# Optimization experiments

Hardware: AMD Instinct MI355X
Metric: run time of the kernel (lower is better)

## Reference

```python
import jax, jax.numpy as jnp
import numpy as np

NEG = -1e9

def mask_from_lens(src_lens, lip_lens, Tx, Ty):
    # [B, Tx, Ty] valid mask
    mx = jnp.arange(Tx)[None, :] < src_lens[:, None]
    my = jnp.arange(Ty)[None, :] < lip_lens[:, None]
    return (mx[:, :, None] & my[:, None, :]).astype(jnp.float32)

def maximum_path(value, mask):
    # Monotonic alignment search (VITS-style). value, mask: [B, Tx, Ty]
    B, Tx, Ty = value.shape
    value = value * mask
    xr = jnp.arange(Tx)[None, :]

    def fwd(v, inp):
        val_j, j = inp
        v0 = jnp.concatenate([jnp.full((B, 1), NEG, value.dtype), v[:, :-1]], axis=1)
        stay = v >= v0                      # True: best prev is same x
        vmax = jnp.where(stay, v, v0)
        vnew = jnp.where(xr <= j, vmax + val_j, NEG)
        return vnew, stay

    val_T = jnp.transpose(value, (2, 0, 1))          # [Ty,B,Tx]
    _, dirs = jax.lax.scan(fwd, jnp.zeros((B, Tx), value.dtype),
                           (val_T, jnp.arange(Ty)))
    mask_T = jnp.transpose(mask, (2, 0, 1)) > 0
    dirs = jnp.where(mask_T, dirs, True)             # padded cols: stay

    idx0 = mask[:, :, 0].sum(1).astype(jnp.int32) - 1  # src_lens - 1
    br = jnp.arange(B)

    def bwd(index, dir_j):
        onehot = jax.nn.one_hot(index, Tx, dtype=value.dtype)
        d = dir_j[br, index]
        return index + d.astype(jnp.int32) - 1, onehot

    _, path = jax.lax.scan(bwd, idx0, dirs, reverse=True)  # [Ty,B,Tx]
    return jnp.transpose(path, (1, 2, 0)) * mask

def setup_inputs() -> dict:
    key = jax.random.key(0)
    k1, k2, k3, k4, k5 = jax.random.split(key, 5)
    B, Ts, Tl, D = 32, 512, 2048, 256
    lip_motion_embedding = jax.random.normal(k1, (B, Tl, D), jnp.float32)
    output_phoneme = jax.random.normal(k2, (B, Ts, D), jnp.float32)
    src_lens = jax.random.randint(k3, (B,), Ts // 2, Ts + 1, jnp.int32)
    lip_lens = jax.random.randint(k4, (B,), Tl // 2, Tl + 1, jnp.int32)
    d_targets = jax.random.randint(k5, (B, Ts), 1, 8, jnp.int32)
    d_targets = jnp.where(jnp.arange(Ts)[None, :] < src_lens[:, None], d_targets, 0)
    return {"lip_motion_embedding": lip_motion_embedding,
            "output_phoneme": output_phoneme,
            "d_targets": d_targets,
            "src_lens": src_lens,
            "lip_lens": lip_lens}

def reference(lip_motion_embedding, output_phoneme, d_targets, src_lens, lip_lens):
    B, Tl, D = lip_motion_embedding.shape
    Ts = output_phoneme.shape[1]

    # mean expansion coefficient
    mean_cof = (d_targets.sum(-1) / lip_lens).mean()

    # normalized similarity  [B, Ts, Tl]
    norm_lip = lip_motion_embedding / jnp.linalg.norm(lip_motion_embedding, axis=2, keepdims=True)
    text_norm_base = jnp.linalg.norm(output_phoneme, axis=2, keepdims=True)
    norm_text = jnp.nan_to_num(output_phoneme / (text_norm_base + 1), nan=1.0)
    similarity = jnp.einsum('bld,bsd->bsl', norm_lip, norm_text)

    # duration targets rescaled to lip frame rate
    cofs = d_targets.sum(1) / lip_lens                      # [B]
    lip_targets = jnp.round(d_targets / cofs[:, None])      # [B, Ts] float
    dif = lip_lens.astype(lip_targets.dtype) - lip_targets.sum(1)
    max_idx = jnp.argmax(lip_targets, axis=1)
    lip_targets = lip_targets.at[jnp.arange(B), max_idx].add(dif)

    # gt_similarity: contiguous segments of ones per phoneme (vectorized scatter)
    lt = lip_targets.astype(jnp.int32)
    ends = jnp.cumsum(lt, axis=1)                           # [B, Ts]
    begins = ends - lt
    kk = jnp.arange(Tl)[None, None, :]
    gt_similarity = ((kk >= begins[:, :, None]) & (kk < ends[:, :, None])).astype(similarity.dtype)

    mask_sim = mask_from_lens(src_lens, lip_lens, Ts, Tl)
    alignment = maximum_path(similarity, mask_sim)
    d_predictions = jax.lax.stop_gradient(alignment.sum(-1)) * mean_cof

    return similarity, gt_similarity, alignment, d_predictions
```

## Files before the change

### kernel.cpp

```cpp
#include <hip/hip_runtime.h>
#include <math.h>

#define BATCH 32
#define TS    512
#define TL    2048
#define DD    256
#define NEGV  -1e9f

#define SIM_OFF   ((size_t)0)
#define GT_OFF    ((size_t)BATCH*TS*TL)
#define ALIGN_OFF ((size_t)2*BATCH*TS*TL)
#define DPRED_OFF ((size_t)3*BATCH*TS*TL)

#define WS_MEAN   0
#define WS_COF    256
#define WS_LSCALE 512
#define WS_TSCALE 262656
#define WS_BEGIN  328192
#define WS_END    393728
#define WS_START2 459264
#define WS_END2   524800
#define WS_DIRS   590848

__global__ __launch_bounds__(256) void norm_kernel(const float* __restrict__ lip,
                                                   const float* __restrict__ phon,
                                                   float* __restrict__ lip_scale,
                                                   float* __restrict__ text_scale) {
    const int wave = threadIdx.x >> 6, lane = threadIdx.x & 63;
    const int row = blockIdx.x * 4 + wave;
    const int NL = BATCH * TL;
    const float* src = (row < NL) ? (lip + (size_t)row * DD)
                                  : (phon + (size_t)(row - NL) * DD);
    float4 q = *(const float4*)(src + lane * 4);
    float ss = q.x*q.x + q.y*q.y + q.z*q.z + q.w*q.w;
    #pragma unroll
    for (int off = 32; off; off >>= 1) ss += __shfl_xor(ss, off);
    if (lane == 0) {
        if (row < NL) lip_scale[row] = 1.0f / sqrtf(ss);
        else          text_scale[row - NL] = 1.0f / (sqrtf(ss) + 1.0f);
    }
}

__global__ __launch_bounds__(512) void prep_kernel(const int* __restrict__ d_targets,
                                                   const int* __restrict__ lip_lens,
                                                   int* __restrict__ begins,
                                                   int* __restrict__ ends,
                                                   float* __restrict__ cof_arr) {
    __shared__ int   si[512];
    __shared__ float sf[512];
    __shared__ int   sx[512];
    const int b = blockIdx.x, t = threadIdx.x;
    const int d = d_targets[b * TS + t];
    const int lipL = lip_lens[b];

    si[t] = d; __syncthreads();
    for (int off = 256; off; off >>= 1) { if (t < off) si[t] += si[t + off]; __syncthreads(); }
    const int sum_d = si[0]; __syncthreads();

    const float cofv = (float)sum_d / (float)lipL;
    float lt = rintf((float)d / cofv);

    sf[t] = lt; __syncthreads();
    for (int off = 256; off; off >>= 1) { if (t < off) sf[t] += sf[t + off]; __syncthreads(); }
    const float sumlt = sf[0]; __syncthreads();
    const float dif = (float)lipL - sumlt;

    sf[t] = lt; sx[t] = t; __syncthreads();
    for (int off = 256; off; off >>= 1) {
        if (t < off) {
            float v2 = sf[t + off]; int i2 = sx[t + off];
            if (v2 > sf[t] || (v2 == sf[t] && i2 < sx[t])) { sf[t] = v2; sx[t] = i2; }
        }
        __syncthreads();
    }
    const int max_idx = sx[0]; __syncthreads();
    if (t == max_idx) lt += dif;
    const int li = (int)lt;

    si[t] = li; __syncthreads();
    for (int off = 1; off < 512; off <<= 1) {
        int add = (t >= off) ? si[t - off] : 0;
        __syncthreads();
        si[t] += add;
        __syncthreads();
    }
    const int e = si[t];
    begins[b * TS + t] = e - li;
    ends[b * TS + t]   = e;
    if (t == 0) cof_arr[b] = cofv;
}

__global__ __launch_bounds__(256) void gemm_kernel(const float* __restrict__ lip,
                                                   const float* __restrict__ phon,
                                                   const float* __restrict__ lip_scale,
                                                   const float* __restrict__ text_scale,
                                                   const int* __restrict__ begins,
                                                   const int* __restrict__ ends,
                                                   float* __restrict__ sim,
                                                   float* __restrict__ gt,
                                                   float* __restrict__ simT) {
    const int b = blockIdx.z, tm = blockIdx.y, tn = blockIdx.x;
    const int t = threadIdx.x;
    __shared__ __align__(16) float As[16][132];
    __shared__ __align__(16) float Bs[16][132];

    const int r = t >> 1, sub = t & 1;
    const int tx = t & 15, ty = t >> 4;

    const float* Ag = phon + ((size_t)(b * TS + tm * 128 + r)) * DD + sub * 8;
    const float* Bg = lip  + ((size_t)(b * TL + tn * 128 + r)) * DD + sub * 8;
    const float sA = text_scale[b * TS + tm * 128 + r];
    const float sB = lip_scale[b * TL + tn * 128 + r];

    float4 ra0 = *(const float4*)(Ag);
    float4 ra1 = *(const float4*)(Ag + 4);
    float4 rb0 = *(const float4*)(Bg);
    float4 rb1 = *(const float4*)(Bg + 4);

    float acc[8][8];
    #pragma unroll
    for (int i = 0; i < 8; ++i)
        #pragma unroll
        for (int j = 0; j < 8; ++j) acc[i][j] = 0.0f;

    for (int kt = 0; kt < 16; ++kt) {
        __syncthreads();
        {
            const float* pa0 = &ra0.x; const float* pa1 = &ra1.x;
            const float* pb0 = &rb0.x; const float* pb1 = &rb1.x;
            #pragma unroll
            for (int kk = 0; kk < 4; ++kk) {
                As[sub * 8 + kk][r]     = pa0[kk] * sA;
                As[sub * 8 + 4 + kk][r] = pa1[kk] * sA;
                Bs[sub * 8 + kk][r]     = pb0[kk] * sB;
                Bs[sub * 8 + 4 + kk][r] = pb1[kk] * sB;
            }
        }
        __syncthreads();
        if (kt < 15) {
            ra0 = *(const float4*)(Ag + (kt + 1) * 16);
            ra1 = *(const float4*)(Ag + (kt + 1) * 16 + 4);
            rb0 = *(const float4*)(Bg + (kt + 1) * 16);
            rb1 = *(const float4*)(Bg + (kt + 1) * 16 + 4);
        }
        #pragma unroll
        for (int kk = 0; kk < 16; ++kk) {
            float4 t0 = *(const float4*)&As[kk][ty * 4];
            float4 t1 = *(const float4*)&As[kk][64 + ty * 4];
            float4 t2 = *(const float4*)&Bs[kk][tx * 4];
            float4 t3 = *(const float4*)&Bs[kk][64 + tx * 4];
            float a[8] = {t0.x, t0.y, t0.z, t0.w, t1.x, t1.y, t1.z, t1.w};
            float bb[8] = {t2.x, t2.y, t2.z, t2.w, t3.x, t3.y, t3.z, t3.w};
            #pragma unroll
            for (int i = 0; i < 8; ++i)
                #pragma unroll
                for (int j = 0; j < 8; ++j)
                    acc[i][j] = fmaf(a[i], bb[j], acc[i][j]);
        }
    }

    const size_t base = (size_t)b * TS * TL;
    #pragma unroll
    for (int mi = 0; mi < 2; ++mi) {
        #pragma unroll
        for (int im = 0; im < 4; ++im) {
            const int srow = tm * 128 + mi * 64 + ty * 4 + im;
            const int ai = mi * 4 + im;
            float* prow = sim + base + (size_t)srow * TL + tn * 128;
            float4 w0 = {acc[ai][0], acc[ai][1], acc[ai][2], acc[ai][3]};
            float4 w1 = {acc[ai][4], acc[ai][5], acc[ai][6], acc[ai][7]};
            *(float4*)(prow + tx * 4) = w0;
            *(float4*)(prow + 64 + tx * 4) = w1;

            const int bg = begins[b * TS + srow], en = ends[b * TS + srow];
            const int l0 = tn * 128 + tx * 4;
            float4 g0, g1;
            g0.x = (l0 + 0 >= bg && l0 + 0 < en) ? 1.f : 0.f;
            g0.y = (l0 + 1 >= bg && l0 + 1 < en) ? 1.f : 0.f;
            g0.z = (l0 + 2 >= bg && l0 + 2 < en) ? 1.f : 0.f;
            g0.w = (l0 + 3 >= bg && l0 + 3 < en) ? 1.f : 0.f;
            g1.x = (l0 + 64 >= bg && l0 + 64 < en) ? 1.f : 0.f;
            g1.y = (l0 + 65 >= bg && l0 + 65 < en) ? 1.f : 0.f;
            g1.z = (l0 + 66 >= bg && l0 + 66 < en) ? 1.f : 0.f;
            g1.w = (l0 + 67 >= bg && l0 + 67 < en) ? 1.f : 0.f;
            float* grow = gt + base + (size_t)srow * TL + tn * 128;
            *(float4*)(grow + tx * 4) = g0;
            *(float4*)(grow + 64 + tx * 4) = g1;
        }
    }

    {
        float* tb = simT + (size_t)b * TL * TS + (size_t)(tn * 128) * TS + tm * 128;
        #pragma unroll
        for (int bj = 0; bj < 8; ++bj) {
            const int lloc = (bj < 4) ? (tx * 4 + bj) : (64 + tx * 4 + (bj - 4));
            float* trow = tb + (size_t)lloc * TS;
            float4 w0 = {acc[0][bj], acc[1][bj], acc[2][bj], acc[3][bj]};
            float4 w1 = {acc[4][bj], acc[5][bj], acc[6][bj], acc[7][bj]};
            *(float4*)(trow + ty * 4) = w0;
            *(float4*)(trow + 64 + ty * 4) = w1;
        }
    }
}

__device__ __forceinline__ void load8T(float4 (&buf)[8][2], const float* simTb, int L, int jb) {
    #pragma unroll
    for (int s = 0; s < 8; ++s) {
        const float* p = simTb + (size_t)(jb + s) * TS + L * 8;
        buf[s][0] = *(const float4*)p;
        buf[s][1] = *(const float4*)(p + 4);
    }
}

template <bool CHK>
__device__ __forceinline__ void step8T(float4 (&buf)[8][2], int jb, float (&v)[8],
                                       unsigned (&w)[8], const float (&xm)[8], int L) {
    #pragma unroll
    for (int s = 0; s < 8; ++s) {
        const int j = jb + s;
        float up = __shfl_up(v[7], 1);
        if (L == 0) up = NEGV;
        const float* vals = (const float*)&buf[s][0];
        #pragma unroll
        for (int i = 7; i >= 0; --i) {
            const float v0 = (i == 0) ? up : v[i - 1];
            const unsigned stay = (v[i] >= v0) ? 1u : 0u;
            const float vm = fmaxf(v[i], v0);
            float nv = fmaf(vals[i], xm[i], vm);
            if (CHK) nv = ((L * 8 + i) <= j) ? nv : NEGV;
            w[i] = w[i] * 2u + stay;
            v[i] = nv;
        }
    }
}

__global__ __launch_bounds__(64) void dp_kernel(const float* __restrict__ simT,
                                                const int* __restrict__ src_lens,
                                                const int* __restrict__ lip_lens,
                                                const float* __restrict__ cof_arr,
                                                float* __restrict__ mean_out,
                                                unsigned* __restrict__ dirs,
                                                int* __restrict__ start2,
                                                int* __restrict__ end2) {
    const int b = blockIdx.x, L = threadIdx.x;
    if (b == 0 && L == 0) {
        float s = 0.f;
        for (int i = 0; i < BATCH; ++i) s += cof_arr[i];
        mean_out[0] = s / 32.0f;
    }
    const int srcL = src_lens[b], lipL = lip_lens[b];
    const float* simTb = simT + (size_t)b * TL * TS;

    float v[8]; unsigned w[8]; float xm[8];
    #pragma unroll
    for (int i = 0; i < 8; ++i) {
        v[i] = 0.f; w[i] = 0u;
        xm[i] = (L * 8 + i < srcL) ? 1.f : 0.f;
    }
    float4 bufA[8][2], bufB[8][2];
    const int jmax = (lipL + 31) & ~31;

    load8T(bufA, simTb, L, 0);
    for (int jb = 0; jb < jmax; jb += 16) {
        load8T(bufB, simTb, L, jb + 8);
        if (jb < 512) step8T<true>(bufA, jb, v, w, xm, L);
        else          step8T<false>(bufA, jb, v, w, xm, L);
        if ((jb & 31) == 24) {
            #pragma unroll
            for (int i = 0; i < 8; ++i) {
                dirs[((size_t)b * TS + L * 8 + i) * 64 + (jb >> 5)] = w[i];
                w[i] = 0u;
            }
        }
        if (jb + 16 < jmax) load8T(bufA, simTb, L, jb + 16);
        if (jb + 8 < 512) step8T<true>(bufB, jb + 8, v, w, xm, L);
        else              step8T<false>(bufB, jb + 8, v, w, xm, L);
        if (((jb + 8) & 31) == 24) {
            #pragma unroll
            for (int i = 0; i < 8; ++i) {
                dirs[((size_t)b * TS + L * 8 + i) * 64 + ((jb + 8) >> 5)] = w[i];
                w[i] = 0u;
            }
        }
    }

    #pragma unroll
    for (int i = 0; i < 8; ++i) {
        start2[b * TS + L + i * 64] = 0;
        end2[b * TS + L + i * 64] = 0;
    }
    asm volatile("s_waitcnt vmcnt(0)" ::: "memory");

    int x = srcL - 1;
    if (L == 0) end2[b * TS + x] = lipL;
    int j = lipL - 1;
    while (x > 0 && j >= 0) {
        const unsigned W = dirs[((size_t)b * TS + x) * 64 + (j >> 5)];
        const int jj = j & 31;
        const unsigned m = (~W) & (0xFFFFFFFFu << (31 - jj));
        if (m == 0u) { j -= jj + 1; continue; }
        const int jp = __builtin_ctz(m);
        const int jprime = (j & ~31) + (31 - jp);
        if (L == 0) { start2[b * TS + x] = jprime; end2[b * TS + x - 1] = jprime; }
        x -= 1; j = jprime - 1;
    }
}

__global__ __launch_bounds__(256) void align_kernel(const int* __restrict__ start2,
                                                    const int* __restrict__ end2,
                                                    const float* __restrict__ mean_cof,
                                                    float* __restrict__ alignOut,
                                                    float* __restrict__ dpred) {
    const int s = blockIdx.x, b = blockIdx.y, t = threadIdx.x;
    const int st = start2[b * TS + s], en = end2[b * TS + s];
    float* row = alignOut + ((size_t)b * TS + s) * TL;
    const int l0 = t * 8;
    float4 r0, r1;
    r0.x = (l0 + 0 >= st && l0 + 0 < en) ? 1.f : 0.f;
    r0.y = (l0 + 1 >= st && l0 + 1 < en) ? 1.f : 0.f;
    r0.z = (l0 + 2 >= st && l0 + 2 < en) ? 1.f : 0.f;
    r0.w = (l0 + 3 >= st && l0 + 3 < en) ? 1.f : 0.f;
    r1.x = (l0 + 4 >= st && l0 + 4 < en) ? 1.f : 0.f;
    r1.y = (l0 + 5 >= st && l0 + 5 < en) ? 1.f : 0.f;
    r1.z = (l0 + 6 >= st && l0 + 6 < en) ? 1.f : 0.f;
    r1.w = (l0 + 7 >= st && l0 + 7 < en) ? 1.f : 0.f;
    *(float4*)(row + l0) = r0;
    *(float4*)(row + l0 + 4) = r1;
    if (t == 0) dpred[b * TS + s] = (float)(en - st) * mean_cof[0];
}

extern "C" void kernel_launch(void* const* d_in, const int* in_sizes, int n_in,
                              void* d_out, int out_size, void* d_ws, size_t ws_size,
                              hipStream_t stream) {
    const float* lip   = (const float*)d_in[0];
    const float* phon  = (const float*)d_in[1];
    const int* d_tg    = (const int*)d_in[2];
    const int* src_l   = (const int*)d_in[3];
    const int* lip_l   = (const int*)d_in[4];
    float* out = (float*)d_out;

    char* ws = (char*)d_ws;
    float*    mean_cof   = (float*)(ws + WS_MEAN);
    float*    cof_arr    = (float*)(ws + WS_COF);
    float*    lip_scale  = (float*)(ws + WS_LSCALE);
    float*    text_scale = (float*)(ws + WS_TSCALE);
    int*      begins     = (int*)(ws + WS_BEGIN);
    int*      ends       = (int*)(ws + WS_END);
    int*      start2     = (int*)(ws + WS_START2);
    int*      end2       = (int*)(ws + WS_END2);
    unsigned* dirs       = (unsigned*)(ws + WS_DIRS);

    float* sim   = out + SIM_OFF;
    float* gt    = out + GT_OFF;
    float* aln   = out + ALIGN_OFF;
    float* dpred = out + DPRED_OFF;

    norm_kernel<<<(BATCH * TL + BATCH * TS) / 4, 256, 0, stream>>>(lip, phon, lip_scale, text_scale);
    prep_kernel<<<BATCH, 512, 0, stream>>>(d_tg, lip_l, begins, ends, cof_arr);
    gemm_kernel<<<dim3(TL / 128, TS / 128, BATCH), 256, 0, stream>>>(lip, phon, lip_scale, text_scale,
                                                                     begins, ends, sim, gt, aln);
    dp_kernel<<<BATCH, 64, 0, stream>>>(aln, src_l, lip_l, cof_arr, mean_cof, dirs, start2, end2);
    align_kernel<<<dim3(TS, BATCH), 256, 0, stream>>>(start2, end2, mean_cof, aln, dpred);
}
```

Baseline: 1.138 ms.

## Keep DP direction bits in LDS and triple-buffer similarity loads

The direction bitmasks from the forward DP now go into a 128KB shared-memory array instead of global workspace, so the serial backtrack reads LDS rather than issuing dependent global loads. The forward loop also switches from double to triple buffering, prefetching 24 columns ahead to hide global-load latency in the latency-bound single-wave DP. This raises register pressure with a third buffer, and the large LDS allocation limits occupancy to one block per CU, which is fine at 32 blocks.

After: 1.011 ms. 11.2% less time.

```diff
diff --git a/kernel.cpp b/kernel.cpp
--- a/kernel.cpp
+++ b/kernel.cpp
@@ -20,7 +20,6 @@
 #define WS_END    393728
 #define WS_START2 459264
 #define WS_END2   524800
-#define WS_DIRS   590848
 
 __global__ __launch_bounds__(256) void norm_kernel(const float* __restrict__ lip,
                                                    const float* __restrict__ phon,
@@ -234,14 +233,15 @@
     }
 }
 
-__global__ __launch_bounds__(64) void dp_kernel(const float* __restrict__ simT,
-                                                const int* __restrict__ src_lens,
-                                                const int* __restrict__ lip_lens,
-                                                const float* __restrict__ cof_arr,
-                                                float* __restrict__ mean_out,
-                                                unsigned* __restrict__ dirs,
-                                                int* __restrict__ start2,
-                                                int* __restrict__ end2) {
+__global__ __launch_bounds__(64, 1) void dp_kernel(const float* __restrict__ simT,
+                                                   const int* __restrict__ src_lens,
+                                                   const int* __restrict__ lip_lens,
+                                                   const float* __restrict__ cof_arr,
+                                                   float* __restrict__ mean_out,
+                                                   int* __restrict__ start2,
+                                                   int* __restrict__ end2) {
+    __shared__ unsigned dirs_lds[64 * 512];
+
     const int b = blockIdx.x, L = threadIdx.x;
     if (b == 0 && L == 0) {
         float s = 0.f;
@@ -257,32 +257,42 @@
         v[i] = 0.f; w[i] = 0u;
         xm[i] = (L * 8 + i < srcL) ? 1.f : 0.f;
     }
-    float4 bufA[8][2], bufB[8][2];
+    float4 bufA[8][2], bufB[8][2], bufC[8][2];
     const int jmax = (lipL + 31) & ~31;
 
     load8T(bufA, simTb, L, 0);
-    for (int jb = 0; jb < jmax; jb += 16) {
-        load8T(bufB, simTb, L, jb + 8);
-        if (jb < 512) step8T<true>(bufA, jb, v, w, xm, L);
-        else          step8T<false>(bufA, jb, v, w, xm, L);
-        if ((jb & 31) == 24) {
-            #pragma unroll
-            for (int i = 0; i < 8; ++i) {
-                dirs[((size_t)b * TS + L * 8 + i) * 64 + (jb >> 5)] = w[i];
-                w[i] = 0u;
-            }
-        }
-        if (jb + 16 < jmax) load8T(bufA, simTb, L, jb + 16);
-        if (jb + 8 < 512) step8T<true>(bufB, jb + 8, v, w, xm, L);
-        else              step8T<false>(bufB, jb + 8, v, w, xm, L);
-        if (((jb + 8) & 31) == 24) {
-            #pragma unroll
-            for (int i = 0; i < 8; ++i) {
-                dirs[((size_t)b * TS + L * 8 + i) * 64 + ((jb + 8) >> 5)] = w[i];
-                w[i] = 0u;
-            }
-        }
-    }
+    load8T(bufB, simTb, L, 8);
+    load8T(bufC, simTb, L, 16);
+
+    int jb = 0;
+#define DP_CHUNK(BUF)                                                          \
+    do {                                                                       \
+        if (jb < 512) step8T<true>(BUF, jb, v, w, xm, L);                      \
+        else          step8T<false>(BUF, jb, v, w, xm, L);                     \
+        if ((jb & 31) == 24) {                                                 \
+            const int wd = jb >> 5;                                            \
+            _Pragma("unroll")                                                  \
+            for (int i = 0; i < 8; ++i) {                                      \
+                dirs_lds[wd * 512 + L * 8 + i] = w[i];                         \
+                w[i] = 0u;                                                     \
+            }                                                                  \
+        }                                                                      \
+        {                                                                      \
+            int jl = jb + 24;                                                  \
+            if (jl > TL - 8) jl = TL - 8;           \
+            load8T(BUF, simTb, L, jl);                                         \
+        }                                                                      \
+        jb += 8;                                                               \
+    } while (0)
+
+    while (jb < jmax) {
+        DP_CHUNK(bufA);
+        if (jb >= jmax) break;
+        DP_CHUNK(bufB);
+        if (jb >= jmax) break;
+        DP_CHUNK(bufC);
+    }
+#undef DP_CHUNK
 
     #pragma unroll
     for (int i = 0; i < 8; ++i) {
@@ -295,7 +305,7 @@
     if (L == 0) end2[b * TS + x] = lipL;
     int j = lipL - 1;
     while (x > 0 && j >= 0) {
-        const unsigned W = dirs[((size_t)b * TS + x) * 64 + (j >> 5)];
+        const unsigned W = dirs_lds[(j >> 5) * 512 + x];
         const int jj = j & 31;
         const unsigned m = (~W) & (0xFFFFFFFFu << (31 - jj));
         if (m == 0u) { j -= jj + 1; continue; }
@@ -348,7 +358,6 @@
     int*      ends       = (int*)(ws + WS_END);
     int*      start2     = (int*)(ws + WS_START2);
     int*      end2       = (int*)(ws + WS_END2);
-    unsigned* dirs       = (unsigned*)(ws + WS_DIRS);
 
     float* sim   = out + SIM_OFF;
     float* gt    = out + GT_OFF;
@@ -359,6 +368,6 @@
     prep_kernel<<<BATCH, 512, 0, stream>>>(d_tg, lip_l, begins, ends, cof_arr);
     gemm_kernel<<<dim3(TL / 128, TS / 128, BATCH), 256, 0, stream>>>(lip, phon, lip_scale, text_scale,
                                                                      begins, ends, sim, gt, aln);
-    dp_kernel<<<BATCH, 64, 0, stream>>>(aln, src_l, lip_l, cof_arr, mean_cof, dirs, start2, end2);
+    dp_kernel<<<BATCH, 64, 0, stream>>>(aln, src_l, lip_l, cof_arr, mean_cof, start2, end2);
     align_kernel<<<dim3(TS, BATCH), 256, 0, stream>>>(start2, end2, mean_cof, aln, dpred);
 }
```

## Wavefront-parallelize DP across four waves with LDS directions; double-buffer GEMM smem

Applied to the files above, without the earlier changes.

The DP kernel now runs four waves per batch, each owning 128 source rows, in a diagonal wavefront over 32-column chunks. Boundary values pass between waves through a small LDS ring, and the direction bitmasks stay in LDS instead of global memory for the backtrack. The GEMM kernel double-buffers its shared-memory tiles so staging and compute need one barrier per k-step instead of two. This targets the latency-bound serial DP with only one wave per batch, at the cost of 128KB of LDS per block, extra per-superstep barriers and more registers.

Result: faster. 1.042 ms (-8.4%).

```diff
diff --git a/kernel.cpp b/kernel.cpp
--- a/kernel.cpp
+++ b/kernel.cpp
@@ -20,7 +20,6 @@
 #define WS_END    393728
 #define WS_START2 459264
 #define WS_END2   524800
-#define WS_DIRS   590848
 
 __global__ __launch_bounds__(256) void norm_kernel(const float* __restrict__ lip,
                                                    const float* __restrict__ phon,
@@ -90,6 +89,44 @@
     if (t == 0) cof_arr[b] = cofv;
 }
 
+#define G_STAGE(B, S)                                                          \
+  { _Pragma("unroll")                                                          \
+    for (int kk = 0; kk < 4; ++kk) {                                           \
+      As[B][sub * 8 + kk][r]     = (&a0[S].x)[kk] * sA;                        \
+      As[B][sub * 8 + 4 + kk][r] = (&a1[S].x)[kk] * sA;                        \
+      Bs[B][sub * 8 + kk][r]     = (&b0[S].x)[kk] * sB;                        \
+      Bs[B][sub * 8 + 4 + kk][r] = (&b1[S].x)[kk] * sB;                        \
+    } }
+
+#define G_COMPUTE(B)                                                           \
+  { _Pragma("unroll")                                                          \
+    for (int kk = 0; kk < 16; ++kk) {                                          \
+      float4 t0 = *(const float4*)&As[B][kk][ty * 4];                          \
+      float4 t1 = *(const float4*)&As[B][kk][64 + ty * 4];                     \
+      float4 t2 = *(const float4*)&Bs[B][kk][tx * 4];                          \
+      float4 t3 = *(const float4*)&Bs[B][kk][64 + tx * 4];                     \
+      float a[8] = {t0.x, t0.y, t0.z, t0.w, t1.x, t1.y, t1.z, t1.w};           \
+      float bbv[8] = {t2.x, t2.y, t2.z, t2.w, t3.x, t3.y, t3.z, t3.w};         \
+      _Pragma("unroll")                                                        \
+      for (int i = 0; i < 8; ++i)                                              \
+        _Pragma("unroll")                                                      \
+        for (int j = 0; j < 8; ++j)                                            \
+          acc[i][j] = fmaf(a[i], bbv[j], acc[i][j]);                           \
+    } }
+
+#define G_ITER(KT, CB, NB)                                                     \
+  {                                                                            \
+    __syncthreads();                                                           \
+    if ((KT) < 14) {                                                           \
+      a0[CB] = *(const float4*)(Ag + ((KT) + 2) * 16);                         \
+      a1[CB] = *(const float4*)(Ag + ((KT) + 2) * 16 + 4);                     \
+      b0[CB] = *(const float4*)(Bg + ((KT) + 2) * 16);                         \
+      b1[CB] = *(const float4*)(Bg + ((KT) + 2) * 16 + 4);                     \
+    }                                                                          \
+    if ((KT) < 15) G_STAGE(NB, NB);                                            \
+    G_COMPUTE(CB);                                                             \
+  }
+
 __global__ __launch_bounds__(256) void gemm_kernel(const float* __restrict__ lip,
                                                    const float* __restrict__ phon,
                                                    const float* __restrict__ lip_scale,
@@ -101,8 +138,8 @@
                                                    float* __restrict__ simT) {
     const int b = blockIdx.z, tm = blockIdx.y, tn = blockIdx.x;
     const int t = threadIdx.x;
-    __shared__ __align__(16) float As[16][132];
-    __shared__ __align__(16) float Bs[16][132];
+    __shared__ __align__(16) float As[2][16][132];
+    __shared__ __align__(16) float Bs[2][16][132];
 
     const int r = t >> 1, sub = t & 1;
     const int tx = t & 15, ty = t >> 4;
@@ -112,10 +149,16 @@
     const float sA = text_scale[b * TS + tm * 128 + r];
     const float sB = lip_scale[b * TL + tn * 128 + r];
 
-    float4 ra0 = *(const float4*)(Ag);
-    float4 ra1 = *(const float4*)(Ag + 4);
-    float4 rb0 = *(const float4*)(Bg);
-    float4 rb1 = *(const float4*)(Bg + 4);
+    float4 a0[2], a1[2], b0[2], b1[2];
+    a0[0] = *(const float4*)(Ag);
+    a1[0] = *(const float4*)(Ag + 4);
+    b0[0] = *(const float4*)(Bg);
+    b1[0] = *(const float4*)(Bg + 4);
+    G_STAGE(0, 0);
+    a0[1] = *(const float4*)(Ag + 16);
+    a1[1] = *(const float4*)(Ag + 16 + 4);
+    b0[1] = *(const float4*)(Bg + 16);
+    b1[1] = *(const float4*)(Bg + 16 + 4);
 
     float acc[8][8];
     #pragma unroll
@@ -123,40 +166,9 @@
         #pragma unroll
         for (int j = 0; j < 8; ++j) acc[i][j] = 0.0f;
 
-    for (int kt = 0; kt < 16; ++kt) {
-        __syncthreads();
-        {
-            const float* pa0 = &ra0.x; const float* pa1 = &ra1.x;
-            const float* pb0 = &rb0.x; const float* pb1 = &rb1.x;
-            #pragma unroll
-            for (int kk = 0; kk < 4; ++kk) {
-                As[sub * 8 + kk][r]     = pa0[kk] * sA;
-                As[sub * 8 + 4 + kk][r] = pa1[kk] * sA;
-                Bs[sub * 8 + kk][r]     = pb0[kk] * sB;
-                Bs[sub * 8 + 4 + kk][r] = pb1[kk] * sB;
-            }
-        }
-        __syncthreads();
-        if (kt < 15) {
-            ra0 = *(const float4*)(Ag + (kt + 1) * 16);
-            ra1 = *(const float4*)(Ag + (kt + 1) * 16 + 4);
-            rb0 = *(const float4*)(Bg + (kt + 1) * 16);
-            rb1 = *(const float4*)(Bg + (kt + 1) * 16 + 4);
-        }
-        #pragma unroll
-        for (int kk = 0; kk < 16; ++kk) {
-            float4 t0 = *(const float4*)&As[kk][ty * 4];
-            float4 t1 = *(const float4*)&As[kk][64 + ty * 4];
-            float4 t2 = *(const float4*)&Bs[kk][tx * 4];
-            float4 t3 = *(const float4*)&Bs[kk][64 + tx * 4];
-            float a[8] = {t0.x, t0.y, t0.z, t0.w, t1.x, t1.y, t1.z, t1.w};
-            float bb[8] = {t2.x, t2.y, t2.z, t2.w, t3.x, t3.y, t3.z, t3.w};
-            #pragma unroll
-            for (int i = 0; i < 8; ++i)
-                #pragma unroll
-                for (int j = 0; j < 8; ++j)
-                    acc[i][j] = fmaf(a[i], bb[j], acc[i][j]);
-        }
+    for (int kt = 0; kt < 16; kt += 2) {
+        G_ITER(kt,     0, 1);
+        G_ITER(kt + 1, 1, 0);
     }
 
     const size_t base = (size_t)b * TS * TL;
@@ -203,106 +215,161 @@
     }
 }
 
-__device__ __forceinline__ void load8T(float4 (&buf)[8][2], const float* simTb, int L, int jb) {
+#define DP_WAVES 4
+
+template <bool CHK>
+__device__ __forceinline__ void dp32(const float (&c0)[32], const float (&c1)[32],
+                                     int j0, int x0, int lane,
+                                     float xm0, float xm1,
+                                     float& v0, float& v1,
+                                     unsigned& w0, unsigned& w1,
+                                     const float (&bw)[32], float (&bbf)[32]) {
     #pragma unroll
-    for (int s = 0; s < 8; ++s) {
-        const float* p = simTb + (size_t)(jb + s) * TS + L * 8;
-        buf[s][0] = *(const float4*)p;
-        buf[s][1] = *(const float4*)(p + 4);
-    }
-}
-
-template <bool CHK>
-__device__ __forceinline__ void step8T(float4 (&buf)[8][2], int jb, float (&v)[8],
-                                       unsigned (&w)[8], const float (&xm)[8], int L) {
-    #pragma unroll
-    for (int s = 0; s < 8; ++s) {
-        const int j = jb + s;
-        float up = __shfl_up(v[7], 1);
-        if (L == 0) up = NEGV;
-        const float* vals = (const float*)&buf[s][0];
+    for (int s = 0; s < 32; ++s) {
+        const int j = j0 + s;
+        float up = __shfl_up(v1, 1);
+        up = (lane == 0) ? bw[s] : up;
+        const float ov0 = v0;
+        const unsigned st0 = (v0 >= up)  ? 1u : 0u;
+        const unsigned st1 = (v1 >= ov0) ? 1u : 0u;
+        float nv0 = fmaf(c0[s], xm0, fmaxf(v0, up));
+        float nv1 = fmaf(c1[s], xm1, fmaxf(v1, ov0));
+        if (CHK) {
+            nv0 = (x0     <= j) ? nv0 : NEGV;
+            nv1 = (x0 + 1 <= j) ? nv1 : NEGV;
+        }
+        w0 = w0 * 2u + st0;
+        w1 = w1 * 2u + st1;
+        bbf[s] = nv1;
+        v0 = nv0; v1 = nv1;
+    }
+}
+
+__device__ __forceinline__ void dp_superstep(const float* __restrict__ simTb,
+                                             unsigned* __restrict__ dirs_lds,
+                                             float* __restrict__ bndl,
+                                             float (&cur0)[32], float (&cur1)[32],
+                                             float (&nxt0)[32], float (&nxt1)[32],
+                                             int T, int k, int lane, int x0, int nchunks,
+                                             float xm0, float xm1,
+                                             float& v0, float& v1,
+                                             unsigned& w0, unsigned& w1) {
+    __syncthreads();
+    const int c  = T - k;
+    const int cp = c + 1;
+    if (cp >= 0 && cp < nchunks) {
+        const int j0p = cp << 5;
         #pragma unroll
-        for (int i = 7; i >= 0; --i) {
-            const float v0 = (i == 0) ? up : v[i - 1];
-            const unsigned stay = (v[i] >= v0) ? 1u : 0u;
-            const float vm = fmaxf(v[i], v0);
-            float nv = fmaf(vals[i], xm[i], vm);
-            if (CHK) nv = ((L * 8 + i) <= j) ? nv : NEGV;
-            w[i] = w[i] * 2u + stay;
-            v[i] = nv;
-        }
-    }
-}
-
-__global__ __launch_bounds__(64) void dp_kernel(const float* __restrict__ simT,
-                                                const int* __restrict__ src_lens,
-                                                const int* __restrict__ lip_lens,
-                                                const float* __restrict__ cof_arr,
-                                                float* __restrict__ mean_out,
-                                                unsigned* __restrict__ dirs,
-                                                int* __restrict__ start2,
-                                                int* __restrict__ end2) {
-    const int b = blockIdx.x, L = threadIdx.x;
-    if (b == 0 && L == 0) {
+        for (int s = 0; s < 32; ++s) {
+            float2 q = *(const float2*)(simTb + (size_t)(j0p + s) * TS + x0);
+            nxt0[s] = q.x; nxt1[s] = q.y;
+        }
+    }
+    if (c >= 0 && c < nchunks) {
+        const int j0 = c << 5;
+        float bw[32];
+        if (k > 0) {
+            const float* br = bndl + (k - 1) * 96;
+            const int r0 = j0 % 96;
+            { float4 bq = *(const float4*)(br + ((r0 + 92) % 96)); bw[0] = bq.w; }
+            #pragma unroll
+            for (int q = 0; q < 8; ++q) {
+                float4 bq = *(const float4*)(br + r0 + (q << 2));
+                bw[4 * q + 1] = bq.x;
+                bw[4 * q + 2] = bq.y;
+                bw[4 * q + 3] = bq.z;
+                if (4 * q + 4 < 32) bw[4 * q + 4] = bq.w;
+            }
+        } else {
+            #pragma unroll
+            for (int s = 0; s < 32; ++s) bw[s] = NEGV;
+        }
+        float bbf[32];
+        if (c < 16) dp32<true >(cur0, cur1, j0, x0, lane, xm0, xm1, v0, v1, w0, w1, bw, bbf);
+        else        dp32<false>(cur0, cur1, j0, x0, lane, xm0, xm1, v0, v1, w0, w1, bw, bbf);
+        if (lane == 63) {
+            float* brw = bndl + k * 96 + (j0 % 96);
+            #pragma unroll
+            for (int q = 0; q < 8; ++q) {
+                float4 w4 = {bbf[4*q], bbf[4*q+1], bbf[4*q+2], bbf[4*q+3]};
+                *(float4*)(brw + 4 * q) = w4;
+            }
+        }
+        dirs_lds[c * 512 + x0]     = w0;
+        dirs_lds[c * 512 + x0 + 1] = w1;
+        w0 = 0u; w1 = 0u;
+    }
+}
+
+__global__ __launch_bounds__(256, 1) void dp_kernel(const float* __restrict__ simT,
+                                                    const int* __restrict__ src_lens,
+                                                    const int* __restrict__ lip_lens,
+                                                    const float* __restrict__ cof_arr,
+                                                    float* __restrict__ mean_out,
+                                                    int* __restrict__ start2,
+                                                    int* __restrict__ end2) {
+    __shared__ unsigned dirs_lds[64 * 512];
+    __shared__ __align__(16) float bndl[DP_WAVES * 96];
+
+    const int b = blockIdx.x, tid = threadIdx.x;
+    const int k = tid >> 6, lane = tid & 63;
+    const int x0 = (k << 7) + (lane << 1);
+
+    if (b == 0 && tid == 0) {
         float s = 0.f;
         for (int i = 0; i < BATCH; ++i) s += cof_arr[i];
         mean_out[0] = s / 32.0f;
     }
+    for (int i = tid; i < DP_WAVES * 96; i += 256) bndl[i] = 0.f;
+
     const int srcL = src_lens[b], lipL = lip_lens[b];
     const float* simTb = simT + (size_t)b * TL * TS;
-
-    float v[8]; unsigned w[8]; float xm[8];
-    #pragma unroll
-    for (int i = 0; i < 8; ++i) {
-        v[i] = 0.f; w[i] = 0u;
-        xm[i] = (L * 8 + i < srcL) ? 1.f : 0.f;
-    }
-    float4 bufA[8][2], bufB[8][2];
-    const int jmax = (lipL + 31) & ~31;
-
-    load8T(bufA, simTb, L, 0);
-    for (int jb = 0; jb < jmax; jb += 16) {
-        load8T(bufB, simTb, L, jb + 8);
-        if (jb < 512) step8T<true>(bufA, jb, v, w, xm, L);
-        else          step8T<false>(bufA, jb, v, w, xm, L);
-        if ((jb & 31) == 24) {
-            #pragma unroll
-            for (int i = 0; i < 8; ++i) {
-                dirs[((size_t)b * TS + L * 8 + i) * 64 + (jb >> 5)] = w[i];
-                w[i] = 0u;
-            }
-        }
-        if (jb + 16 < jmax) load8T(bufA, simTb, L, jb + 16);
-        if (jb + 8 < 512) step8T<true>(bufB, jb + 8, v, w, xm, L);
-        else              step8T<false>(bufB, jb + 8, v, w, xm, L);
-        if (((jb + 8) & 31) == 24) {
-            #pragma unroll
-            for (int i = 0; i < 8; ++i) {
-                dirs[((size_t)b * TS + L * 8 + i) * 64 + ((jb + 8) >> 5)] = w[i];
-                w[i] = 0u;
-            }
-        }
-    }
-
-    #pragma unroll
-    for (int i = 0; i < 8; ++i) {
-        start2[b * TS + L + i * 64] = 0;
-        end2[b * TS + L + i * 64] = 0;
-    }
+    const int nchunks = (lipL + 31) >> 5;
+
+    const float xm0 = (x0     < srcL) ? 1.f : 0.f;
+    const float xm1 = (x0 + 1 < srcL) ? 1.f : 0.f;
+    float v0 = 0.f, v1 = 0.f;
+    unsigned w0 = 0u, w1 = 0u;
+
+    float curA0[32], curA1[32], curB0[32], curB1[32];
+    if (k == 0) {
+        #pragma unroll
+        for (int s = 0; s < 32; ++s) {
+            float2 q = *(const float2*)(simTb + (size_t)s * TS + x0);
+            curA0[s] = q.x; curA1[s] = q.y;
+        }
+    }
+
+    const int tot = nchunks + DP_WAVES - 1;
+    for (int t = 0; t < tot; t += 2) {
+        dp_superstep(simTb, dirs_lds, bndl, curA0, curA1, curB0, curB1,
+                     t, k, lane, x0, nchunks, xm0, xm1, v0, v1, w0, w1);
+        if (t + 1 < tot)
+            dp_superstep(simTb, dirs_lds, bndl, curB0, curB1, curA0, curA1,
+                         t + 1, k, lane, x0, nchunks, xm0, xm1, v0, v1, w0, w1);
+    }
+
+    start2[b * TS + tid]       = 0;
+    end2[b * TS + tid]         = 0;
+    start2[b * TS + tid + 256] = 0;
+    end2[b * TS + tid + 256]   = 0;
     asm volatile("s_waitcnt vmcnt(0)" ::: "memory");
-
-    int x = srcL - 1;
-    if (L == 0) end2[b * TS + x] = lipL;
-    int j = lipL - 1;
-    while (x > 0 && j >= 0) {
-        const unsigned W = dirs[((size_t)b * TS + x) * 64 + (j >> 5)];
-        const int jj = j & 31;
-        const unsigned m = (~W) & (0xFFFFFFFFu << (31 - jj));
-        if (m == 0u) { j -= jj + 1; continue; }
-        const int jp = __builtin_ctz(m);
-        const int jprime = (j & ~31) + (31 - jp);
-        if (L == 0) { start2[b * TS + x] = jprime; end2[b * TS + x - 1] = jprime; }
-        x -= 1; j = jprime - 1;
+    __syncthreads();
+
+    if (k == 0) {
+        int x = srcL - 1;
+        if (lane == 0) end2[b * TS + x] = lipL;
+        int j = lipL - 1;
+        while (x > 0 && j >= 0) {
+            const unsigned W = dirs_lds[(j >> 5) * 512 + x];
+            const int jj = j & 31;
+            const unsigned m = (~W) & (0xFFFFFFFFu << (31 - jj));
+            if (m == 0u) { j -= jj + 1; continue; }
+            const int jp = __builtin_ctz(m);
+            const int jprime = (j & ~31) + (31 - jp);
+            if (lane == 0) { start2[b * TS + x] = jprime; end2[b * TS + x - 1] = jprime; }
+            x -= 1; j = jprime - 1;
+        }
     }
 }
 
@@ -348,7 +415,6 @@
     int*      ends       = (int*)(ws + WS_END);
     int*      start2     = (int*)(ws + WS_START2);
     int*      end2       = (int*)(ws + WS_END2);
-    unsigned* dirs       = (unsigned*)(ws + WS_DIRS);
 
     float* sim   = out + SIM_OFF;
     float* gt    = out + GT_OFF;
@@ -359,6 +425,6 @@
     prep_kernel<<<BATCH, 512, 0, stream>>>(d_tg, lip_l, begins, ends, cof_arr);
     gemm_kernel<<<dim3(TL / 128, TS / 128, BATCH), 256, 0, stream>>>(lip, phon, lip_scale, text_scale,
                                                                      begins, ends, sim, gt, aln);
-    dp_kernel<<<BATCH, 64, 0, stream>>>(aln, src_l, lip_l, cof_arr, mean_cof, dirs, start2, end2);
+    dp_kernel<<<BATCH, 256, 0, stream>>>(aln, src_l, lip_l, cof_arr, mean_cof, start2, end2);
     align_kernel<<<dim3(TS, BATCH), 256, 0, stream>>>(start2, end2, mean_cof, aln, dpred);
 }
```
